# Kernel tuning notes

Measured on AMD Instinct MI355X. Metric: run time of the kernel, lower is better.

The kernel has to match this reference:

```python
import jax, jax.numpy as jnp
import numpy as np

BATCH, SEQ, EMBED = 8, 1024, 2048
HEADS, LATENT = 16, 512
HEAD_DIM = EMBED // HEADS            # 128
NOPE = HEAD_DIM // 4                 # 32 (qk_rope_dim=96 is even, no adjust)
ROPE_D = HEAD_DIM - NOPE             # 96
THETA = 10000.0


def _rope_tables(seq_len):
    # matches torch: freqs over arange(0, rope_dim, 2)/rope_dim
    freqs = 1.0 / THETA ** (jnp.arange(0, ROPE_D, 2, dtype=jnp.float32) / ROPE_D)
    emb = jnp.arange(seq_len, dtype=jnp.float32)[:, None] * freqs[None, :]  # [S, ROPE_D//2]
    return jnp.cos(emb), jnp.sin(emb)


def _apply_rope(x, cos, sin):
    # x: [B,H,S,D]; cos/sin: [S,D//2]. NOTE: original concatenates halves (non-interleaved output).
    xe, xo = x[..., ::2], x[..., 1::2]
    return jnp.concatenate([xe * cos - xo * sin, xo * cos + xe * sin], axis=-1)


def setup_inputs() -> dict:
    key = jax.random.key(0)
    ks = jax.random.split(key, 5)
    x = jax.random.normal(ks[0], (BATCH, SEQ, EMBED), jnp.float32)
    Wq = jax.random.normal(ks[1], (EMBED, EMBED), jnp.float32) * 0.02
    Wkv_down = jax.random.normal(ks[2], (EMBED, LATENT), jnp.float32) * 0.02
    Wk_up = jax.random.normal(ks[3], (LATENT, EMBED), jnp.float32) * 0.02
    Wv_up = jax.random.normal(ks[4], (LATENT, EMBED), jnp.float32) * 0.02
    return {"x": x, "Wq": Wq, "Wkv_down": Wkv_down, "Wk_up": Wk_up, "Wv_up": Wv_up}


def reference(x, Wq, Wkv_down, Wk_up, Wv_up):
    B, S, E = x.shape
    # projections (weights stored [in, out], equivalent to nn.Linear math)
    q = (x @ Wq).reshape(B, S, HEADS, HEAD_DIM).transpose(0, 2, 1, 3)   # [B,H,S,D]
    q_nope, q_rope = q[..., :NOPE], q[..., NOPE:]
    c_kv = x @ Wkv_down                                                  # [B,S,latent]
    k = (c_kv @ Wk_up).reshape(B, S, HEADS, HEAD_DIM).transpose(0, 2, 1, 3)
    v = (c_kv @ Wv_up).reshape(B, S, HEADS, HEAD_DIM).transpose(0, 2, 1, 3)
    k_nope, k_rope = k[..., :NOPE], k[..., NOPE:]

    cos, sin = _rope_tables(S)
    q_rope = _apply_rope(q_rope, cos, sin)
    k_rope = _apply_rope(k_rope, cos, sin)

    qf = jnp.concatenate([q_nope, q_rope], axis=-1)
    kf = jnp.concatenate([k_nope, k_rope], axis=-1)

    scale = jnp.float32(1.0 / np.sqrt(HEAD_DIM))
    scores = jnp.einsum('bhqd,bhkd->bhqk', qf, kf) * scale
    causal = jnp.triu(jnp.ones((S, S), dtype=bool), k=1)  # past_length=0
    scores = jnp.where(causal, -jnp.inf, scores)
    weights = jax.nn.softmax(scores, axis=-1)
    out = jnp.einsum('bhqk,bhkd->bhqd', weights, v)
    return out.transpose(0, 2, 1, 3).reshape(B, S, E)
```

## Files before the change

kernel.cpp:

```cpp
#include <hip/hip_runtime.h>
#include <stdint.h>

typedef unsigned short u16;
typedef __bf16 bf16x8 __attribute__((ext_vector_type(8)));
typedef float    f32x4 __attribute__((ext_vector_type(4)));
typedef unsigned short u16x8 __attribute__((ext_vector_type(8)));
typedef unsigned short u16x4 __attribute__((ext_vector_type(4)));

#define BB 8
#define SS 1024
#define EE 2048
#define HH 16
#define DD 128

__device__ __forceinline__ u16 f2bf(float f){
  union { float f; unsigned u; } v; v.f = f;
  unsigned r = v.u + 0x7FFFu + ((v.u >> 16) & 1u);
  return (u16)(r >> 16);
}
__device__ __forceinline__ float bf2f(u16 h){
  union { unsigned u; float f; } v; v.u = ((unsigned)h) << 16;
  return v.f;
}
__device__ __forceinline__ bf16x8 ld8(const u16* p){
  return __builtin_bit_cast(bf16x8, *(const u16x8*)p);
}

typedef __attribute__((address_space(1))) const unsigned int gas_u32;
typedef __attribute__((address_space(3))) unsigned int las_u32;
__device__ __forceinline__ void g2l16(const u16* g, u16* l){
  __builtin_amdgcn_global_load_lds((gas_u32*)g, (las_u32*)l, 16, 0, 0);
}

#define BARRIER() asm volatile("s_barrier" ::: "memory")
#define VMC(n)    asm volatile("s_waitcnt vmcnt(" #n ")" ::: "memory")

__global__ __launch_bounds__(256) void cvt_f32_bf16(const float* __restrict__ in,
                                                    u16* __restrict__ out, int n){
  int i = (blockIdx.x*256 + threadIdx.x)*8;
  if (i >= n) return;
  float4 v0 = *(const float4*)(in + i);
  float4 v1 = *(const float4*)(in + i + 4);
  u16x8 o;
  o[0]=f2bf(v0.x); o[1]=f2bf(v0.y); o[2]=f2bf(v0.z); o[3]=f2bf(v0.w);
  o[4]=f2bf(v1.x); o[5]=f2bf(v1.y); o[6]=f2bf(v1.z); o[7]=f2bf(v1.w);
  *(u16x8*)(out + i) = o;
}

__global__ __launch_bounds__(256) void transposeW(const float* __restrict__ W,
                                                  u16* __restrict__ Wt, int K, int N){
  __shared__ float t[32][33];
  int c = threadIdx.x & 31, r = threadIdx.x >> 5;
  int bx = blockIdx.x, by = blockIdx.y;
  #pragma unroll
  for (int i = 0; i < 32; i += 8)
    t[r+i][c] = W[(size_t)(by*32 + r + i)*N + bx*32 + c];
  __syncthreads();
  #pragma unroll
  for (int i = 0; i < 32; i += 8)
    Wt[(size_t)(bx*32 + r + i)*K + by*32 + c] = f2bf(t[c][r+i]);
}

__global__ __launch_bounds__(256) void rope_tables(float* __restrict__ cosb,
                                                   float* __restrict__ sinb){
  int i = blockIdx.x*256 + threadIdx.x;
  if (i >= SS*48) return;
  int s = i / 48, j = i % 48;
  float freq = powf(10000.0f, -((float)(2*j)) / 96.0f);
  float e = (float)s * freq;
  cosb[i] = cosf(e);
  sinb[i] = sinf(e);
}

__global__ __launch_bounds__(256) void rope_apply2(u16* __restrict__ qp,
                                                   u16* __restrict__ kp,
                                                   const float* __restrict__ cosb,
                                                   const float* __restrict__ sinb){
  u16* base = blockIdx.y ? kp : qp;
  int t = blockIdx.x*256 + threadIdx.x;
  int row = t >> 4, h = t & 15, s = row & (SS-1);
  u16* p = base + (size_t)row*EE + h*DD + 32;
  float e[48], o[48];
  #pragma unroll
  for (int c = 0; c < 12; c++){
    u16x8 v = *(const u16x8*)(p + c*8);
    #pragma unroll
    for (int j = 0; j < 4; j++){
      e[c*4 + j] = bf2f(v[2*j]);
      o[c*4 + j] = bf2f(v[2*j+1]);
    }
  }
  u16 ob[96];
  #pragma unroll
  for (int j = 0; j < 48; j++){
    float cs = cosb[s*48 + j], sn = sinb[s*48 + j];
    ob[j]      = f2bf(e[j]*cs - o[j]*sn);
    ob[48 + j] = f2bf(o[j]*cs + e[j]*sn);
  }
  #pragma unroll
  for (int c = 0; c < 12; c++)
    *(u16x8*)(p + c*8) = *(const u16x8*)(ob + c*8);
}

__global__ __launch_bounds__(256) void gemm_bt(const u16* __restrict__ A,
    const u16* __restrict__ Bt, u16* __restrict__ C, int M, int N, int K){
  __shared__ u16 Al[128*32];
  __shared__ u16 Bl[128*32];
  const int tid = threadIdx.x;
  const int lane = tid & 63, w = tid >> 6;
  const int wr = w >> 1, wc = w & 1;
  const int l15 = lane & 15, l4 = lane >> 4;
  const int bm = blockIdx.y*128, bn = blockIdx.x*128;
  const int srow = tid >> 2;
  const int skc  = (tid & 3) * 8;
  const u16* ga = A  + (size_t)(bm + srow)*K + skc;
  const u16* gb = Bt + (size_t)(bn + srow)*K + skc;
  u16* la = Al + w*512;
  u16* lb = Bl + w*512;
  f32x4 acc[4][4] = {};
  for (int k0 = 0; k0 < K; k0 += 32){
    __syncthreads();
    g2l16(ga + k0,          la);
    g2l16(ga + 64*K + k0,   la + 2048);
    g2l16(gb + k0,          lb);
    g2l16(gb + 64*K + k0,   lb + 2048);
    __syncthreads();
    bf16x8 af[4], bfr[4];
    #pragma unroll
    for (int m = 0; m < 4; m++) af[m]  = ld8(Al + (wr*64 + m*16 + l15)*32 + l4*8);
    #pragma unroll
    for (int n = 0; n < 4; n++) bfr[n] = ld8(Bl + (wc*64 + n*16 + l15)*32 + l4*8);
    #pragma unroll
    for (int m = 0; m < 4; m++)
      #pragma unroll
      for (int n = 0; n < 4; n++)
        acc[m][n] = __builtin_amdgcn_mfma_f32_16x16x32_bf16(af[m], bfr[n], acc[m][n], 0, 0, 0);
  }
  #pragma unroll
  for (int m = 0; m < 4; m++)
    #pragma unroll
    for (int n = 0; n < 4; n++)
      #pragma unroll
      for (int r = 0; r < 4; r++){
        int row = bm + wr*64 + m*16 + l4*4 + r;
        int col = bn + wc*64 + n*16 + l15;
        C[(size_t)row*N + col] = f2bf(acc[m][n][r]);
      }
}

#define AFR(buf, mf, ks) ld8(&AL[buf][wr][((mf)*16 + l15)*64 + ((((ks)*4 + l4) ^ r7) << 3)])
#define BFR(buf, nf, ks) ld8(&BL[buf][wc>>1][(((wc&1)*64 + (nf)*16 + l15))*64 + ((((ks)*4 + l4) ^ r7) << 3)])

#define STAGE_A(buf, h, kt) stage2(aRow, (h), (kt), K, &AL[buf][h][0], wj0)
#define STAGE_B(buf, h, kt) stage2(bRow, (h), (kt), K, &BL[buf][h][0], wj0)

__device__ __forceinline__ void stage2(const u16* rowbase, int h, int kt, int K,
                                       u16* lds, int wj0){
  const u16* g = rowbase + (size_t)h*128*K + kt*64;
  g2l16(g,               lds + wj0*512);
  g2l16(g + (size_t)8*K, lds + wj0*512 + 512);
}

#define PHASE(buf, q, LOADB, STAGE, VM) do{                                        \
  bf16x8 a00 = AFR(buf, 2*(q)  , 0);                                              \
  bf16x8 a01 = AFR(buf, 2*(q)  , 1);                                              \
  bf16x8 a10 = AFR(buf, 2*(q)+1, 0);                                              \
  bf16x8 a11 = AFR(buf, 2*(q)+1, 1);                                              \
  if (LOADB){                                                                      \
    _Pragma("unroll")                                                              \
    for (int nf = 0; nf < 4; nf++){ bq[nf][0]=BFR(buf,nf,0); bq[nf][1]=BFR(buf,nf,1); } \
  }                                                                                \
  STAGE;                                                                           \
  if (VM) VMC(4);                                                                  \
  BARRIER();                                                                       \
  __builtin_amdgcn_s_setprio(1);                                                   \
  _Pragma("unroll")                                                                \
  for (int nf = 0; nf < 4; nf++){                                                  \
    acc[2*(q)][nf]   = __builtin_amdgcn_mfma_f32_16x16x32_bf16(a00, bq[nf][0], acc[2*(q)][nf],0,0,0);   \
    acc[2*(q)+1][nf] = __builtin_amdgcn_mfma_f32_16x16x32_bf16(a10, bq[nf][0], acc[2*(q)+1][nf],0,0,0); \
  }                                                                                \
  _Pragma("unroll")                                                                \
  for (int nf = 0; nf < 4; nf++){                                                  \
    acc[2*(q)][nf]   = __builtin_amdgcn_mfma_f32_16x16x32_bf16(a01, bq[nf][1], acc[2*(q)][nf],0,0,0);   \
    acc[2*(q)+1][nf] = __builtin_amdgcn_mfma_f32_16x16x32_bf16(a11, bq[nf][1], acc[2*(q)+1][nf],0,0,0); \
  }                                                                                \
  __builtin_amdgcn_s_setprio(0);                                                   \
  BARRIER();                                                                       \
  __builtin_amdgcn_sched_barrier(0);                                               \
}while(0)

__global__ __launch_bounds__(512, 2) void gemm8(const u16* __restrict__ A,
    const u16* __restrict__ Bt, u16* __restrict__ C0, u16* __restrict__ C1,
    int K, int Nout, int nsplit, int vt){
  __shared__ u16 AL[2][2][128*64];
  __shared__ u16 BL[2][2][128*64];
  const int tid = threadIdx.x, lane = tid & 63, w = tid >> 6;
  const int wr = w >> 2, wc = w & 3;
  const int l15 = lane & 15, l4 = lane >> 4;
  const int r7 = l15 & 7;
  const int bm = blockIdx.y*256, bn = blockIdx.x*256;
  const int wj0 = w*2;
  const int cswz = (lane & 7) ^ (lane >> 3);
  const u16* aRow = A  + (size_t)(bm + wj0*8 + (lane>>3))*K + cswz*8;
  const u16* bRow = Bt + (size_t)(bn + wj0*8 + (lane>>3))*K + cswz*8;

  const int nkt = K >> 6;
  const int niter = nkt >> 1;

  STAGE_A(0, 0, 0); STAGE_A(0, 1, 0);
  STAGE_B(0, 0, 0); STAGE_B(0, 1, 0);
  STAGE_B(1, 0, 1); STAGE_B(1, 1, 1);
  VMC(4);
  BARRIER();

  f32x4 acc[8][4] = {};
  bf16x8 bq[4][2];

  for (int it = 0; it < niter; ++it){
    const int kto = 2*it + 1;
    int kt2 = 2*it + 2; if (kt2 >= nkt) kt2 -= nkt;
    int kt3 = 2*it + 3; if (kt3 >= nkt) kt3 -= nkt;
    PHASE(0, 0, 1, STAGE_A(1, 0, kto), 0);
    PHASE(0, 1, 0, STAGE_A(1, 1, kto), 0);
    PHASE(0, 2, 0, STAGE_B(0, 0, kt2), 0);
    PHASE(0, 3, 0, STAGE_B(0, 1, kt2), 1);
    PHASE(1, 0, 1, STAGE_A(0, 0, kt2), 0);
    PHASE(1, 1, 0, STAGE_A(0, 1, kt2), 0);
    PHASE(1, 2, 0, STAGE_B(1, 0, kt3), 0);
    PHASE(1, 3, 0, STAGE_B(1, 1, kt3), 1);
  }
  asm volatile("s_waitcnt vmcnt(0)" ::: "memory");

  if (vt && bn >= nsplit){
    const int bcol = bn - nsplit;
    #pragma unroll
    for (int mf = 0; mf < 8; mf++)
      #pragma unroll
      for (int nf = 0; nf < 4; nf++){
        int row0 = bm + wr*128 + mf*16 + l4*4;
        int col  = bcol + wc*64 + nf*16 + l15;
        int bh = (row0 >> 10)*16 + (col >> 7);
        int d  = col & 127;
        int s  = row0 & 1023;
        u16x4 pk;
        #pragma unroll
        for (int r = 0; r < 4; r++) pk[r] = f2bf(acc[mf][nf][r]);
        *(u16x4*)(C1 + (((size_t)(bh*128 + d)) << 10) + s) = pk;
      }
  } else {
    u16* Cd = (bn < nsplit) ? C0 : C1;
    const int bcol = (bn < nsplit) ? bn : bn - nsplit;
    #pragma unroll
    for (int mf = 0; mf < 8; mf++)
      #pragma unroll
      for (int nf = 0; nf < 4; nf++)
        #pragma unroll
        for (int r = 0; r < 4; r++){
          int row = bm + wr*128 + mf*16 + l4*4 + r;
          int col = bcol + wc*64 + nf*16 + l15;
          Cd[(size_t)row*Nout + col] = f2bf(acc[mf][nf][r]);
        }
  }
}

__global__ __launch_bounds__(512) void attn(const u16* __restrict__ qp,
                                            const u16* __restrict__ kp,
                                            const u16* __restrict__ vpT,
                                            float* __restrict__ out){
  __shared__ u16 Kl[2][64*128];
  __shared__ u16 Vl[2][128*64];
  __shared__ u16 Pl[8][16*64];
  const int tid = threadIdx.x, lane = tid & 63, w = tid >> 6;
  const int l15 = lane & 15, l4 = lane >> 4;
  const int qt = 7 - blockIdx.y;
  const int bh = blockIdx.x;
  const int b = bh >> 4, h = bh & 15;
  const int qbase = qt*128;
  const int qmin = qbase + w*16;
  const float c = 0.12751920700948998f;
  const float THR = 62.7f;

  const size_t rowq = (size_t)(b*SS + qmin + l15)*EE + h*DD;
  bf16x8 qf[4];
  #pragma unroll
  for (int kk = 0; kk < 4; kk++) qf[kk] = ld8(qp + rowq + kk*32 + l4*8);
  #pragma unroll
  for (int kk = 0; kk < 4; kk++) asm volatile("" : "+v"(qf[kk]));

  f32x4 ao[8] = {};
  float mi[4], li[4];
  #pragma unroll
  for (int r = 0; r < 4; r++){ mi[r] = -3e38f; li[r] = 0.0f; }

  const int ntiles = 2*qt + 2;

  const int krow = w*8 + (lane>>4);
  const int kcol = ((lane & 15) ^ (krow & 7)) << 3;
  const int vd   = w*16 + (lane>>3);
  const int vcc  = lane & 7;

  #pragma unroll
  for (int q = 0; q < 2; q++){
    int r = w*8 + q*4 + (lane>>4);
    g2l16(kp + (size_t)(b*SS + r)*EE + h*DD + (((lane&15) ^ (r&7))<<3),
          &Kl[0][0] + w*1024 + q*512);
    int d = w*16 + q*8 + (lane>>3);
    g2l16(vpT + (size_t)(bh*DD + d)*SS + ((vcc ^ (d&7))<<3),
          &Vl[0][0] + w*1024 + q*512);
  }

  for (int t = 0; t < ntiles; t++){
    const int kv0 = t*64;
    const int buf = t & 1;
    {
      const int kvn = (t + 1 < ntiles) ? kv0 + 64 : kv0;
      #pragma unroll
      for (int q = 0; q < 2; q++){
        int r = w*8 + q*4 + (lane>>4);
        g2l16(kp + (size_t)(b*SS + kvn + r)*EE + h*DD + (((lane&15) ^ (r&7))<<3),
              &Kl[buf^1][0] + w*1024 + q*512);
        int d = w*16 + q*8 + (lane>>3);
        g2l16(vpT + (size_t)(bh*DD + d)*SS + kvn + ((vcc ^ (d&7))<<3),
              &Vl[buf^1][0] + w*1024 + q*512);
      }
    }
    VMC(4);
    BARRIER();

    if (kv0 <= qmin + 15){
      float sv[4][4];
      __builtin_amdgcn_s_setprio(1);
      #pragma unroll
      for (int nt = 0; nt < 4; nt++){
        f32x4 sacc = {};
        #pragma unroll
        for (int kk = 0; kk < 4; kk++){
          bf16x8 kf = ld8(&Kl[buf][0] + (nt*16 + l15)*128 + (((kk*4 + l4) ^ (l15&7))<<3));
          sacc = __builtin_amdgcn_mfma_f32_16x16x32_bf16(qf[kk], kf, sacc, 0, 0, 0);
        }
        #pragma unroll
        for (int r = 0; r < 4; r++) sv[nt][r] = sacc[r];
      }
      __builtin_amdgcn_s_setprio(0);
      if (kv0 + 63 > qmin){
        #pragma unroll
        for (int nt = 0; nt < 4; nt++)
          #pragma unroll
          for (int r = 0; r < 4; r++){
            int qg = qmin + l4*4 + r;
            int kg_ = kv0 + nt*16 + l15;
            if (kg_ > qg) sv[nt][r] = -3e38f;
          }
      }
      float mx[4];
      int need = 0;
      #pragma unroll
      for (int r = 0; r < 4; r++){
        float m0 = fmaxf(fmaxf(sv[0][r], sv[1][r]), fmaxf(sv[2][r], sv[3][r]));
        #pragma unroll
        for (int off = 1; off < 16; off <<= 1) m0 = fmaxf(m0, __shfl_xor(m0, off));
        mx[r] = m0;
        need |= (m0 > mi[r] + THR);
      }
      if (__any(need)){
        #pragma unroll
        for (int r = 0; r < 4; r++){
          float mnew = fmaxf(mi[r], mx[r]);
          float alpha = __builtin_amdgcn_exp2f((mi[r] - mnew)*c);
          mi[r] = mnew;
          li[r] *= alpha;
          #pragma unroll
          for (int n8 = 0; n8 < 8; n8++) ao[n8][r] *= alpha;
        }
      }
      float pout[4][4];
      #pragma unroll
      for (int r = 0; r < 4; r++){
        float mnc = mi[r]*c;
        float rs = 0.0f;
        #pragma unroll
        for (int nt = 0; nt < 4; nt++){
          float pv = __builtin_amdgcn_exp2f(__builtin_fmaf(sv[nt][r], c, -mnc));
          pout[nt][r] = pv; rs += pv;
        }
        #pragma unroll
        for (int off = 1; off < 16; off <<= 1) rs += __shfl_xor(rs, off);
        li[r] += rs;
      }
      #pragma unroll
      for (int nt = 0; nt < 4; nt++)
        #pragma unroll
        for (int r = 0; r < 4; r++){
          int row = l4*4 + r;
          Pl[w][row*64 + (((nt*2 + (l15>>3)) ^ (row&7))<<3) + (l15&7)] = f2bf(pout[nt][r]);
        }
      __builtin_amdgcn_s_setprio(1);
      #pragma unroll
      for (int kk = 0; kk < 2; kk++){
        bf16x8 pa = ld8(&Pl[w][l15*64 + (((kk*4 + l4) ^ (l15&7))<<3)]);
        #pragma unroll
        for (int n8 = 0; n8 < 8; n8++){
          bf16x8 vf = ld8(&Vl[buf][0] + (n8*16 + l15)*64 + (((kk*4 + l4) ^ (l15&7))<<3));
          ao[n8] = __builtin_amdgcn_mfma_f32_16x16x32_bf16(pa, vf, ao[n8], 0, 0, 0);
        }
      }
      __builtin_amdgcn_s_setprio(0);
    }
    BARRIER();
  }
  asm volatile("s_waitcnt vmcnt(0)" ::: "memory");

  #pragma unroll
  for (int r = 0; r < 4; r++){
    float inv = 1.0f / li[r];
    size_t orow = (size_t)(b*SS + qmin + l4*4 + r)*EE + h*DD;
    #pragma unroll
    for (int n8 = 0; n8 < 8; n8++)
      out[orow + n8*16 + l15] = ao[n8][r]*inv;
  }
}

extern "C" void kernel_launch(void* const* d_in, const int* in_sizes, int n_in,
                              void* d_out, int out_size, void* d_ws, size_t ws_size,
                              hipStream_t stream){
  const float* x    = (const float*)d_in[0];
  const float* Wq   = (const float*)d_in[1];
  const float* Wkvd = (const float*)d_in[2];
  const float* Wku  = (const float*)d_in[3];
  const float* Wvu  = (const float*)d_in[4];
  float* out = (float*)d_out;
  char* ws = (char*)d_ws;

  u16*   xb    = (u16*)  (ws);
  u16*   WqT   = (u16*)  (ws +  33554432);
  u16*   WkvdT = (u16*)  (ws +  41943040);
  u16*   WkuT  = (u16*)  (ws +  44040192);
  u16*   WvuT  = (u16*)  (ws +  46137344);
  float* cosb  = (float*)(ws +  48234496);
  float* sinb  = (float*)(ws +  48431104);
  u16*   qp    = (u16*)  (ws +  48627712);
  u16*   ckv   = (u16*)  (ws +  82182144);
  u16*   kp    = (u16*)  (ws +  90570752);
  u16*   vpT   = (u16*)  (ws + 124125184);

  cvt_f32_bf16<<<(BB*SS*EE)/(256*8), 256, 0, stream>>>(x, xb, BB*SS*EE);
  transposeW<<<dim3(EE/32,  EE/32), 256, 0, stream>>>(Wq,   WqT,   EE,  EE);
  transposeW<<<dim3(512/32, EE/32), 256, 0, stream>>>(Wkvd, WkvdT, EE,  512);
  transposeW<<<dim3(EE/32, 512/32), 256, 0, stream>>>(Wku,  WkuT,  512, EE);
  transposeW<<<dim3(EE/32, 512/32), 256, 0, stream>>>(Wvu,  WvuT,  512, EE);
  rope_tables<<<(SS*48 + 255)/256, 256, 0, stream>>>(cosb, sinb);

  gemm8<<<dim3(EE/256, (BB*SS)/256), 512, 0, stream>>>(xb, WqT, qp, qp, EE, EE, EE, 0);
  gemm_bt<<<dim3(512/128, (BB*SS)/128), 256, 0, stream>>>(xb, WkvdT, ckv, BB*SS, 512, EE);
  gemm8<<<dim3(4096/256, (BB*SS)/256), 512, 0, stream>>>(ckv, WkuT, kp, vpT, 512, EE, EE, 1);

  rope_apply2<<<dim3((BB*SS*HH)/256, 2), 256, 0, stream>>>(qp, kp, cosb, sinb);

  attn<<<dim3(BB*HH, SS/128), 512, 0, stream>>>(qp, kp, vpT, out);
}
```

Before: 341.3 us.

## Transpose attention MFMA operands so each lane owns one query row

Swaps the MFMA operand order for both QK^T and PV, so each lane's accumulator holds one query row spread across keys or head dims. Row max and row sum now need only two cross-lane shuffles instead of four per row, and softmax state becomes one scalar per lane. P is written to LDS as packed 4-element vectors into a narrower padded buffer, processed one 32-key chunk at a time. The output is stored as float4 vectors instead of scalar stores. The aim is to cut shuffle, LDS-store and softmax bookkeeping overhead, at the cost of a new padded P layout that may cause bank conflicts.

```diff
diff --git a/kernel.cpp b/kernel.cpp
--- a/kernel.cpp
+++ b/kernel.cpp
@@ -263,13 +263,15 @@
   }
 }
 
+#define PLW 40
+
 __global__ __launch_bounds__(512) void attn(const u16* __restrict__ qp,
                                             const u16* __restrict__ kp,
                                             const u16* __restrict__ vpT,
                                             float* __restrict__ out){
   __shared__ u16 Kl[2][64*128];
   __shared__ u16 Vl[2][128*64];
-  __shared__ u16 Pl[8][16*64];
+  __shared__ u16 Pl[8][16*PLW];
   const int tid = threadIdx.x, lane = tid & 63, w = tid >> 6;
   const int l15 = lane & 15, l4 = lane >> 4;
   const int qt = 7 - blockIdx.y;
@@ -277,10 +279,11 @@
   const int b = bh >> 4, h = bh & 15;
   const int qbase = qt*128;
   const int qmin = qbase + w*16;
+  const int qg = qmin + l15;
   const float c = 0.12751920700948998f;
   const float THR = 62.7f;
 
-  const size_t rowq = (size_t)(b*SS + qmin + l15)*EE + h*DD;
+  const size_t rowq = (size_t)(b*SS + qg)*EE + h*DD;
   bf16x8 qf[4];
   #pragma unroll
   for (int kk = 0; kk < 4; kk++) qf[kk] = ld8(qp + rowq + kk*32 + l4*8);
@@ -288,16 +291,10 @@
   for (int kk = 0; kk < 4; kk++) asm volatile("" : "+v"(qf[kk]));
 
   f32x4 ao[8] = {};
-  float mi[4], li[4];
-  #pragma unroll
-  for (int r = 0; r < 4; r++){ mi[r] = -3e38f; li[r] = 0.0f; }
+  float mi = -3e38f, li = 0.0f;
 
   const int ntiles = 2*qt + 2;
-
-  const int krow = w*8 + (lane>>4);
-  const int kcol = ((lane & 15) ^ (krow & 7)) << 3;
-  const int vd   = w*16 + (lane>>3);
-  const int vcc  = lane & 7;
+  const int vcc = lane & 7;
 
   #pragma unroll
   for (int q = 0; q < 2; q++){
@@ -336,7 +333,7 @@
         #pragma unroll
         for (int kk = 0; kk < 4; kk++){
           bf16x8 kf = ld8(&Kl[buf][0] + (nt*16 + l15)*128 + (((kk*4 + l4) ^ (l15&7))<<3));
-          sacc = __builtin_amdgcn_mfma_f32_16x16x32_bf16(qf[kk], kf, sacc, 0, 0, 0);
+          sacc = __builtin_amdgcn_mfma_f32_16x16x32_bf16(kf, qf[kk], sacc, 0, 0, 0);
         }
         #pragma unroll
         for (int r = 0; r < 4; r++) sv[nt][r] = sacc[r];
@@ -347,76 +344,68 @@
         for (int nt = 0; nt < 4; nt++)
           #pragma unroll
           for (int r = 0; r < 4; r++){
-            int qg = qmin + l4*4 + r;
-            int kg_ = kv0 + nt*16 + l15;
-            if (kg_ > qg) sv[nt][r] = -3e38f;
+            int kg = kv0 + nt*16 + l4*4 + r;
+            if (kg > qg) sv[nt][r] = -3e38f;
           }
       }
-      float mx[4];
-      int need = 0;
-      #pragma unroll
-      for (int r = 0; r < 4; r++){
-        float m0 = fmaxf(fmaxf(sv[0][r], sv[1][r]), fmaxf(sv[2][r], sv[3][r]));
-        #pragma unroll
-        for (int off = 1; off < 16; off <<= 1) m0 = fmaxf(m0, __shfl_xor(m0, off));
-        mx[r] = m0;
-        need |= (m0 > mi[r] + THR);
-      }
-      if (__any(need)){
+      float mx = sv[0][0];
+      #pragma unroll
+      for (int nt = 0; nt < 4; nt++)
+        #pragma unroll
+        for (int r = 0; r < 4; r++) mx = fmaxf(mx, sv[nt][r]);
+      mx = fmaxf(mx, __shfl_xor(mx, 16));
+      mx = fmaxf(mx, __shfl_xor(mx, 32));
+      if (__any(mx > mi + THR)){
+        float mnew = fmaxf(mi, mx);
+        float alpha = __builtin_amdgcn_exp2f((mi - mnew)*c);
+        li *= alpha;
+        #pragma unroll
+        for (int n8 = 0; n8 < 8; n8++) ao[n8] *= alpha;
+        mi = mnew;
+      }
+      const float mnc = mi*c;
+      float pout[4][4];
+      float rs = 0.0f;
+      #pragma unroll
+      for (int nt = 0; nt < 4; nt++)
         #pragma unroll
         for (int r = 0; r < 4; r++){
-          float mnew = fmaxf(mi[r], mx[r]);
-          float alpha = __builtin_amdgcn_exp2f((mi[r] - mnew)*c);
-          mi[r] = mnew;
-          li[r] *= alpha;
-          #pragma unroll
-          for (int n8 = 0; n8 < 8; n8++) ao[n8][r] *= alpha;
-        }
-      }
-      float pout[4][4];
-      #pragma unroll
-      for (int r = 0; r < 4; r++){
-        float mnc = mi[r]*c;
-        float rs = 0.0f;
-        #pragma unroll
-        for (int nt = 0; nt < 4; nt++){
           float pv = __builtin_amdgcn_exp2f(__builtin_fmaf(sv[nt][r], c, -mnc));
           pout[nt][r] = pv; rs += pv;
         }
-        #pragma unroll
-        for (int off = 1; off < 16; off <<= 1) rs += __shfl_xor(rs, off);
-        li[r] += rs;
-      }
-      #pragma unroll
-      for (int nt = 0; nt < 4; nt++)
-        #pragma unroll
-        for (int r = 0; r < 4; r++){
-          int row = l4*4 + r;
-          Pl[w][row*64 + (((nt*2 + (l15>>3)) ^ (row&7))<<3) + (l15&7)] = f2bf(pout[nt][r]);
+      rs += __shfl_xor(rs, 16);
+      rs += __shfl_xor(rs, 32);
+      li += rs;
+      #pragma unroll
+      for (int kk = 0; kk < 2; kk++){
+        #pragma unroll
+        for (int ntl = 0; ntl < 2; ntl++){
+          int nt = kk*2 + ntl;
+          u16x4 pk;
+          #pragma unroll
+          for (int r = 0; r < 4; r++) pk[r] = f2bf(pout[nt][r]);
+          *(u16x4*)(&Pl[w][l15*PLW + ntl*16 + l4*4]) = pk;
         }
-      __builtin_amdgcn_s_setprio(1);
-      #pragma unroll
-      for (int kk = 0; kk < 2; kk++){
-        bf16x8 pa = ld8(&Pl[w][l15*64 + (((kk*4 + l4) ^ (l15&7))<<3)]);
+        bf16x8 pa = ld8(&Pl[w][l15*PLW + l4*8]);
+        __builtin_amdgcn_s_setprio(1);
         #pragma unroll
         for (int n8 = 0; n8 < 8; n8++){
           bf16x8 vf = ld8(&Vl[buf][0] + (n8*16 + l15)*64 + (((kk*4 + l4) ^ (l15&7))<<3));
-          ao[n8] = __builtin_amdgcn_mfma_f32_16x16x32_bf16(pa, vf, ao[n8], 0, 0, 0);
+          ao[n8] = __builtin_amdgcn_mfma_f32_16x16x32_bf16(vf, pa, ao[n8], 0, 0, 0);
         }
-      }
-      __builtin_amdgcn_s_setprio(0);
+        __builtin_amdgcn_s_setprio(0);
+      }
     }
     BARRIER();
   }
   asm volatile("s_waitcnt vmcnt(0)" ::: "memory");
 
-  #pragma unroll
-  for (int r = 0; r < 4; r++){
-    float inv = 1.0f / li[r];
-    size_t orow = (size_t)(b*SS + qmin + l4*4 + r)*EE + h*DD;
-    #pragma unroll
-    for (int n8 = 0; n8 < 8; n8++)
-      out[orow + n8*16 + l15] = ao[n8][r]*inv;
+  const float inv = 1.0f / li;
+  const size_t orow = (size_t)(b*SS + qg)*EE + h*DD;
+  #pragma unroll
+  for (int n8 = 0; n8 < 8; n8++){
+    f32x4 o = ao[n8]*inv;
+    *(float4*)(out + orow + n8*16 + l4*4) = __builtin_bit_cast(float4, o);
   }
 }
 
```

Result: faster. 306.8 us (-10.1%).
